# Optimization experiments

Measured on AMD Instinct MI355X. Metric: run time of the kernel, lower is better.

Reference implementation:

```python
import jax, jax.numpy as jnp
import numpy as np
import math

B, S, D = 16, 256, 1024   # batch, seq (= s_model), d_model
HP, HC = 16, 8
DK, SK = D // HP, S // HC
EPS = 1e-6


def setup_inputs() -> dict:
    key = jax.random.key(0)
    ks = jax.random.split(key, 3)
    x = jax.random.normal(ks[0], (B, S, D), dtype=jnp.float32)
    Wp = jax.random.normal(ks[1], (3, D, D), dtype=jnp.float32) * 0.02  # (in,out)
    bp = jnp.zeros((3, D), dtype=jnp.float32)
    Wc = jax.random.normal(ks[2], (4, S, S), dtype=jnp.float32) * 0.02  # (in,out)
    bc = jnp.zeros((4, S), dtype=jnp.float32)
    a_p = jnp.ones((D,), dtype=jnp.float32)
    b_p = jnp.zeros((D,), dtype=jnp.float32)
    a_c = jnp.ones((S,), dtype=jnp.float32)
    b_c = jnp.zeros((S,), dtype=jnp.float32)
    return {"x": x, "Wp": Wp, "bp": bp, "Wc": Wc, "bc": bc,
            "a_p": a_p, "b_p": b_p, "a_c": a_c, "b_c": b_c}


def _std(x, axis):
    # torch .std(): unbiased (ddof=1)
    return jnp.std(x, axis=axis, keepdims=True, ddof=1)


def _attn(q, k, v):
    # q,k,v: [B, H, T, dk]; dropout is identity (eval)
    scores = jnp.einsum('bhtd,bhsd->bhts', q, k) / math.sqrt(q.shape[-1])
    p = jax.nn.softmax(scores, axis=-1)
    return jnp.einsum('bhts,bhsd->bhtd', p, v)


def reference(x, Wp, bp, Wc, bc, a_p, b_p, a_c, b_c):
    nb = x.shape[0]
    # ---- LayerNorm over channels (norm_p) ----
    mean = jnp.mean(x, axis=-1, keepdims=True)
    xp = a_p * (x - mean) / (_std(x, -1) + EPS) + b_p            # [B,S,D]
    # ---- positional attention over sequence ----
    qkv = jnp.einsum('bsd,nde->nbse', xp, Wp) + bp[:, None, None, :]
    q, k, v = [t.reshape(nb, S, HP, DK).transpose(0, 2, 1, 3) for t in qkv]
    xp = _attn(q, k, v).transpose(0, 2, 1, 3).reshape(nb, S, D)  # [B,S,D]
    # ---- LayerNorm_C: stats over sequence dim, affine indexed by seq ----
    mean_c = jnp.mean(xp, axis=-2, keepdims=True)                # [B,1,D]
    xc = a_c[:, None] * (xp - mean_c) / (_std(xp, -2) + EPS) + b_c[:, None]
    # ---- channel attention: channels are tokens, head dim SK ----
    xt = xc.transpose(0, 2, 1)                                    # [B,D,S]
    qkvc = jnp.einsum('bds,nse->nbde', xt, Wc[:3]) + bc[:3, None, None, :]
    qc, kc, vc = [t.reshape(nb, D, HC, SK).transpose(0, 2, 1, 3) for t in qkvc]
    xcatt = _attn(qc, kc, vc).transpose(0, 2, 1, 3).reshape(nb, D, S)  # [B,D,S]
    out = jnp.einsum('bds,se->bde', xcatt, Wc[3]) + bc[3]         # [B,D,S]
    return out.transpose(0, 2, 1)                                  # [B,S,D]
```

## Files before the change

### kernel.cpp

```cpp
#include <hip/hip_runtime.h>
#include <hip/hip_bf16.h>
#include <math.h>

#define B_ 16
#define S_ 256
#define D_ 1024
#define HP_ 16
#define DK_ 64
#define HC_ 8
#define SK_ 32
#define EPS_ 1e-6f

#define ALPHA_P 0.42466089973135876f
#define ALPHA_C 0.50500991942f

typedef __attribute__((ext_vector_type(8))) short short8v;
typedef __attribute__((ext_vector_type(4))) float f32x4;

__device__ __forceinline__ float bf2f(unsigned short h) {
    return __uint_as_float((unsigned)h << 16);
}
__device__ __forceinline__ ushort2 f2bf2(float a, float b) {
    __hip_bfloat162 h = __float22bfloat162_rn(make_float2(a, b));
    union { __hip_bfloat162 h2; ushort2 u2; } cv;
    cv.h2 = h;
    return cv.u2;
}
__device__ __forceinline__ float exp2_fast(float x) {
    float r;
    asm("v_exp_f32 %0, %1\n\ts_nop 0" : "=v"(r) : "v"(x));
    return r;
}
__device__ __forceinline__ void ldlds16(const unsigned short* g, unsigned short* l) {
    const unsigned int* gp = reinterpret_cast<const unsigned int*>(g);
    auto* lp = reinterpret_cast<__attribute__((address_space(3))) unsigned int*>(
        reinterpret_cast<uintptr_t>(l));
    __builtin_amdgcn_global_load_lds(gp, lp, 16, 0, 0);
}

__global__ __launch_bounds__(256) void k1_ln_p(
    const float* __restrict__ x, const float* __restrict__ a_p,
    const float* __restrict__ b_p, unsigned short* __restrict__ xh,
    unsigned short* __restrict__ xl)
{
    const int row = blockIdx.x;
    const float4* xr = (const float4*)(x + (size_t)row * D_);
    const int tid = threadIdx.x;
    float4 v = xr[tid];
    float s  = v.x + v.y + v.z + v.w;
    float sq = v.x*v.x + v.y*v.y + v.z*v.z + v.w*v.w;
    #pragma unroll
    for (int off = 32; off > 0; off >>= 1) {
        s  += __shfl_down(s, off);
        sq += __shfl_down(sq, off);
    }
    __shared__ float red[8];
    const int wid = tid >> 6, lane = tid & 63;
    if (lane == 0) { red[wid] = s; red[4 + wid] = sq; }
    __syncthreads();
    if (tid == 0) {
        float S0 = red[0] + red[1] + red[2] + red[3];
        float Q0 = red[4] + red[5] + red[6] + red[7];
        float mean = S0 / (float)D_;
        float var  = fmaxf((Q0 - (float)D_ * mean * mean) / (float)(D_ - 1), 0.0f);
        red[0] = mean;
        red[1] = 1.0f / (sqrtf(var) + EPS_);
    }
    __syncthreads();
    const float mean = red[0], inv = red[1];
    float4 a = ((const float4*)a_p)[tid];
    float4 b = ((const float4*)b_p)[tid];
    float o0 = a.x * (v.x - mean) * inv + b.x;
    float o1 = a.y * (v.y - mean) * inv + b.y;
    float o2 = a.z * (v.z - mean) * inv + b.z;
    float o3 = a.w * (v.w - mean) * inv + b.w;
    ushort2 h01 = f2bf2(o0, o1), h23 = f2bf2(o2, o3);
    ushort2 l01 = f2bf2(o0 - bf2f(h01.x), o1 - bf2f(h01.y));
    ushort2 l23 = f2bf2(o2 - bf2f(h23.x), o3 - bf2f(h23.y));
    ushort4 hv, lv;
    hv.x = h01.x; hv.y = h01.y; hv.z = h23.x; hv.w = h23.y;
    lv.x = l01.x; lv.y = l01.y; lv.z = l23.x; lv.w = l23.y;
    *(ushort4*)&xh[(size_t)row * D_ + tid*4] = hv;
    *(ushort4*)&xl[(size_t)row * D_ + tid*4] = lv;
}

__global__ __launch_bounds__(256) void tsplit(
    const float* __restrict__ W, unsigned short* __restrict__ Th,
    unsigned short* __restrict__ Tl, int K, int N)
{
    const int z = blockIdx.z;
    W  += (size_t)z * K * N;
    Th += (size_t)z * K * N;
    Tl += (size_t)z * K * N;
    const int k0 = blockIdx.x * 64, n0 = blockIdx.y * 64;
    __shared__ float tile[64][65];
    const int ix = threadIdx.x & 63, iy = threadIdx.x >> 6;
    #pragma unroll
    for (int u = 0; u < 16; u++) {
        const int kk = iy*16 + u;
        tile[kk][ix] = W[(size_t)(k0+kk)*N + n0 + ix];
    }
    __syncthreads();
    #pragma unroll
    for (int u = 0; u < 16; u += 2) {
        const int nn0 = iy*16 + u, nn1 = nn0 + 1;
        const float v0 = tile[ix][nn0], v1 = tile[ix][nn1];
        ushort2 h2 = f2bf2(v0, v1);
        ushort2 l2 = f2bf2(v0 - bf2f(h2.x), v1 - bf2f(h2.y));
        Th[(size_t)(n0+nn0)*K + k0 + ix] = h2.x;
        Th[(size_t)(n0+nn1)*K + k0 + ix] = h2.y;
        Tl[(size_t)(n0+nn0)*K + k0 + ix] = l2.x;
        Tl[(size_t)(n0+nn1)*K + k0 + ix] = l2.y;
    }
}

template<int OUTMODE, int Z>
__global__ __launch_bounds__(256) void mm_mfma(
    const unsigned short* __restrict__ Ah, const unsigned short* __restrict__ Al,
    const unsigned short* __restrict__ Bh, const unsigned short* __restrict__ Bl,
    const float* __restrict__ bias, void* __restrict__ Cout1,
    void* __restrict__ Cout2,
    int M, int N, int K, long sB, long sBias, long sC, long loff, int TB,
    float alpha, int zsplit, int zobase, int lognx)
{
    const int nwg = gridDim.x * gridDim.y;
    const int chunk = nwg >> 3;
    const int flat = blockIdx.x + gridDim.x * blockIdx.y;
    const int logical = (flat & 7) * chunk + (flat >> 3);
    const int bx = logical & ((1 << lognx) - 1);
    const int by = logical >> lognx;
    const int n0 = bx * 128, m0 = by * 128;
    __shared__ __align__(16) unsigned short Ash[2][2][128*32];
    __shared__ __align__(16) unsigned short Bsh[2][Z][2][128*32];
    const int tid = threadIdx.x;
    const int wave = tid >> 6, lane = tid & 63;
    const int wm = wave & 1, wn = wave >> 1;
    const int lrow = lane & 15, quad = lane >> 4;
    size_t gaOff[2], gbOff[2];
    int cb[2];
    #pragma unroll
    for (int j = 0; j < 2; j++) {
        const int p = wave*128 + j*64 + lane;
        const int row = p >> 2;
        const int cc = (p & 3) ^ ((row >> 1) & 3);
        gaOff[j] = (size_t)(m0 + row) * K + cc*8;
        gbOff[j] = (size_t)(n0 + row) * K + cc*8;
        cb[j] = (wave*128 + j*64) * 8;
    }
    int aFr[4], bFr[4];
    #pragma unroll
    for (int i = 0; i < 4; i++) {
        const int ra = wm*64 + i*16 + lrow;
        aFr[i] = ((ra << 2) | (quad ^ ((ra >> 1) & 3))) * 8;
        const int rb = wn*64 + i*16 + lrow;
        bFr[i] = ((rb << 2) | (quad ^ ((rb >> 1) & 3))) * 8;
    }
    f32x4 acc[Z][4][4];
    #pragma unroll
    for (int z = 0; z < Z; z++)
        #pragma unroll
        for (int j = 0; j < 4; j++) {
            const float bv = bias[(size_t)(z + zobase) * sBias + n0 + wn*64 + j*16 + lrow];
            #pragma unroll
            for (int i = 0; i < 4; i++) {
                acc[z][i][j][0] = bv; acc[z][i][j][1] = bv;
                acc[z][i][j][2] = bv; acc[z][i][j][3] = bv;
            }
        }
    #pragma unroll
    for (int j = 0; j < 2; j++) {
        ldlds16(Ah + gaOff[j], &Ash[0][0][cb[j]]);
        ldlds16(Al + gaOff[j], &Ash[0][1][cb[j]]);
        #pragma unroll
        for (int z = 0; z < Z; z++) {
            ldlds16(Bh + (size_t)z * sB + gbOff[j], &Bsh[0][z][0][cb[j]]);
            ldlds16(Bl + (size_t)z * sB + gbOff[j], &Bsh[0][z][1][cb[j]]);
        }
    }
    const int NT = K >> 5;
    for (int kt = 0; kt < NT; kt++) {
        const int cur = kt & 1;
        asm volatile("s_waitcnt vmcnt(0)" ::: "memory");
        asm volatile("s_barrier" ::: "memory");
        if (kt + 1 < NT) {
            const int kk = (kt + 1) * 32;
            #pragma unroll
            for (int j = 0; j < 2; j++) {
                ldlds16(Ah + gaOff[j] + kk, &Ash[cur^1][0][cb[j]]);
                ldlds16(Al + gaOff[j] + kk, &Ash[cur^1][1][cb[j]]);
                #pragma unroll
                for (int z = 0; z < Z; z++) {
                    ldlds16(Bh + (size_t)z * sB + gbOff[j] + kk, &Bsh[cur^1][z][0][cb[j]]);
                    ldlds16(Bl + (size_t)z * sB + gbOff[j] + kk, &Bsh[cur^1][z][1][cb[j]]);
                }
            }
        }
        short8v ahf[4], alf[4];
        #pragma unroll
        for (int i = 0; i < 4; i++) {
            ahf[i] = *(const short8v*)&Ash[cur][0][aFr[i]];
            alf[i] = *(const short8v*)&Ash[cur][1][aFr[i]];
        }
        #pragma unroll
        for (int z = 0; z < Z; z++) {
            short8v bhf[4], blf[4];
            #pragma unroll
            for (int j = 0; j < 4; j++) {
                bhf[j] = *(const short8v*)&Bsh[cur][z][0][bFr[j]];
                blf[j] = *(const short8v*)&Bsh[cur][z][1][bFr[j]];
            }
            #pragma unroll
            for (int i = 0; i < 4; i++) {
                #pragma unroll
                for (int j = 0; j < 4; j++) {
                    acc[z][i][j] = __builtin_amdgcn_mfma_f32_16x16x32_bf16(ahf[i], bhf[j], acc[z][i][j], 0, 0, 0);
                    acc[z][i][j] = __builtin_amdgcn_mfma_f32_16x16x32_bf16(ahf[i], blf[j], acc[z][i][j], 0, 0, 0);
                    acc[z][i][j] = __builtin_amdgcn_mfma_f32_16x16x32_bf16(alf[i], bhf[j], acc[z][i][j], 0, 0, 0);
                }
            }
        }
    }
    #pragma unroll
    for (int z = 0; z < Z; z++) {
        const int zeff = z + zobase;
        #pragma unroll
        for (int i = 0; i < 4; i++) {
            const int mrow = m0 + wm*64 + i*16 + quad*4;
            #pragma unroll
            for (int j = 0; j < 4; j++) {
                const int ncol = n0 + wn*64 + j*16 + lrow;
                if (OUTMODE == 1) {
                    if (zeff < zsplit) {
                        unsigned short* Ch = (unsigned short*)Cout1 + (size_t)zeff * sC;
                        unsigned short* Cl = Ch + loff;
                        #pragma unroll
                        for (int r = 0; r < 4; r += 2) {
                            const float v0 = acc[z][i][j][r] * alpha;
                            const float v1 = acc[z][i][j][r+1] * alpha;
                            ushort2 h2 = f2bf2(v0, v1);
                            ushort2 l2 = f2bf2(v0 - bf2f(h2.x), v1 - bf2f(h2.y));
                            Ch[(size_t)(mrow + r    ) * N + ncol] = h2.x;
                            Ch[(size_t)(mrow + r + 1) * N + ncol] = h2.y;
                            Cl[(size_t)(mrow + r    ) * N + ncol] = l2.x;
                            Cl[(size_t)(mrow + r + 1) * N + ncol] = l2.y;
                        }
                    } else {
                        unsigned short* Ch = (unsigned short*)Cout2;
                        unsigned short* Cl = Ch + loff;
                        const int bidx = mrow / TB, t0 = mrow % TB;
                        const size_t ad = (size_t)bidx * N * TB + (size_t)ncol * TB + t0;
                        const float v0 = acc[z][i][j][0], v1 = acc[z][i][j][1];
                        const float v2 = acc[z][i][j][2], v3 = acc[z][i][j][3];
                        ushort2 h01 = f2bf2(v0, v1), h23 = f2bf2(v2, v3);
                        ushort2 l01 = f2bf2(v0 - bf2f(h01.x), v1 - bf2f(h01.y));
                        ushort2 l23 = f2bf2(v2 - bf2f(h23.x), v3 - bf2f(h23.y));
                        ushort4 hv, lv;
                        hv.x = h01.x; hv.y = h01.y; hv.z = h23.x; hv.w = h23.y;
                        lv.x = l01.x; lv.y = l01.y; lv.z = l23.x; lv.w = l23.y;
                        *(ushort4*)&Ch[ad] = hv;
                        *(ushort4*)&Cl[ad] = lv;
                    }
                } else {
                    float* C = (float*)Cout2;
                    const int bidx = mrow / TB, t0 = mrow % TB;
                    f32x4 a4 = acc[z][i][j];
                    *(float4*)&C[((size_t)bidx * N + ncol) * TB + t0] = *(float4*)&a4;
                }
            }
        }
    }
}

__global__ __launch_bounds__(256) void k3_mfma(
    const unsigned short* __restrict__ qh, const unsigned short* __restrict__ ql,
    const unsigned short* __restrict__ kh, const unsigned short* __restrict__ kl,
    const unsigned short* __restrict__ vth, const unsigned short* __restrict__ vtl,
    float* __restrict__ out)
{
    const int flat = blockIdx.x + (blockIdx.y << 2) + (blockIdx.z << 6);
    const int logical = ((flat & 7) << 7) | (flat >> 3);
    const int m0 = (logical & 3) * 64;
    const int h  = (logical >> 2) & 15;
    const int b  = logical >> 6;
    const int hoff = h * DK_;
    const size_t rowb = (size_t)b * S_;
    __shared__ __align__(16) unsigned short Ksh[2][64*64], Ksl[2][64*64];
    __shared__ __align__(16) unsigned short VTh[2][64*64], VTl[2][64*64];
    __shared__ __align__(16) unsigned short Ps[64][72];
    const int tid = threadIdx.x;
    const int w = tid >> 6, lane = tid & 63;
    const int lrow = lane & 15, quad = lane >> 4;
    short8v bqh[2], bql[2];
    #pragma unroll
    for (int ks = 0; ks < 2; ks++) {
        const size_t qb = (rowb + m0 + w*16 + lrow) * D_ + hoff + ks*32 + quad*8;
        bqh[ks] = *(const short8v*)&qh[qb];
        bql[ks] = *(const short8v*)&ql[qb];
    }
    size_t kOff[2], vOff[2];
    int cb[2];
    #pragma unroll
    for (int j = 0; j < 2; j++) {
        const int p = w*128 + j*64 + lane;
        const int row = p >> 3;
        const int cc = (p & 7) ^ (row & 7);
        kOff[j] = (rowb + row) * D_ + hoff + cc*8;
        vOff[j] = ((size_t)b * D_ + hoff + row) * S_ + cc*8;
        cb[j] = (w*128 + j*64) * 8;
    }
    f32x4 o[4] = {};
    float lacc = 0.f;
    #pragma unroll
    for (int j = 0; j < 2; j++) {
        ldlds16(kh  + kOff[j], &Ksh[0][cb[j]]);
        ldlds16(kl  + kOff[j], &Ksl[0][cb[j]]);
        ldlds16(vth + vOff[j], &VTh[0][cb[j]]);
        ldlds16(vtl + vOff[j], &VTl[0][cb[j]]);
    }
    for (int kt = 0; kt < 4; kt++) {
        const int cur = kt & 1;
        asm volatile("s_waitcnt vmcnt(0)" ::: "memory");
        asm volatile("s_barrier" ::: "memory");
        if (kt < 3) {
            const int n01 = (kt + 1) * 64;
            #pragma unroll
            for (int j = 0; j < 2; j++) {
                ldlds16(kh  + kOff[j] + (size_t)n01 * D_, &Ksh[cur^1][cb[j]]);
                ldlds16(kl  + kOff[j] + (size_t)n01 * D_, &Ksl[cur^1][cb[j]]);
                ldlds16(vth + vOff[j] + n01,              &VTh[cur^1][cb[j]]);
                ldlds16(vtl + vOff[j] + n01,              &VTl[cur^1][cb[j]]);
            }
        }
        f32x4 sa[4] = {};
        #pragma unroll
        for (int ks = 0; ks < 2; ks++) {
            #pragma unroll
            for (int jk = 0; jk < 4; jk++) {
                const int r = jk*16 + lrow, c = ks*4 + quad;
                const int off = ((r << 3) | (c ^ (r & 7))) * 8;
                short8v akh = *(const short8v*)&Ksh[cur][off];
                short8v akl = *(const short8v*)&Ksl[cur][off];
                sa[jk] = __builtin_amdgcn_mfma_f32_16x16x32_bf16(akh, bqh[ks], sa[jk], 0, 0, 0);
                sa[jk] = __builtin_amdgcn_mfma_f32_16x16x32_bf16(akl, bqh[ks], sa[jk], 0, 0, 0);
                sa[jk] = __builtin_amdgcn_mfma_f32_16x16x32_bf16(akh, bql[ks], sa[jk], 0, 0, 0);
            }
        }
        #pragma unroll
        for (int jk = 0; jk < 4; jk++) {
            float p0 = exp2_fast(sa[jk][0]);
            float p1 = exp2_fast(sa[jk][1]);
            float p2 = exp2_fast(sa[jk][2]);
            float p3 = exp2_fast(sa[jk][3]);
            lacc += (p0 + p1) + (p2 + p3);
            ushort2 p01 = f2bf2(p0, p1), p23 = f2bf2(p2, p3);
            ushort4 ph;
            ph.x = p01.x; ph.y = p01.y; ph.z = p23.x; ph.w = p23.y;
            *(ushort4*)&Ps[w*16 + lrow][jk*16 + quad*4] = ph;
        }
        #pragma unroll
        for (int ks = 0; ks < 2; ks++) {
            short8v ap = *(const short8v*)&Ps[w*16 + lrow][ks*32 + quad*8];
            #pragma unroll
            for (int nf = 0; nf < 4; nf++) {
                const int r = nf*16 + lrow, c = ks*4 + quad;
                const int off = ((r << 3) | (c ^ (r & 7))) * 8;
                short8v vH = *(const short8v*)&VTh[cur][off];
                short8v vL = *(const short8v*)&VTl[cur][off];
                o[nf] = __builtin_amdgcn_mfma_f32_16x16x32_bf16(ap, vH, o[nf], 0, 0, 0);
                o[nf] = __builtin_amdgcn_mfma_f32_16x16x32_bf16(ap, vL, o[nf], 0, 0, 0);
            }
        }
    }
    lacc += __shfl_xor(lacc, 16);
    lacc += __shfl_xor(lacc, 32);
    #pragma unroll
    for (int r = 0; r < 4; r++) {
        const float linv = 1.0f / __shfl(lacc, quad*4 + r);
        #pragma unroll
        for (int nf = 0; nf < 4; nf++)
            out[(rowb + m0 + w*16 + quad*4 + r) * D_ + hoff + nf*16 + lrow] =
                o[nf][r] * linv;
    }
}

__global__ __launch_bounds__(256) void k6_mfma(
    const unsigned short* __restrict__ qch, const unsigned short* __restrict__ qcl,
    const unsigned short* __restrict__ kch, const unsigned short* __restrict__ kcl,
    const unsigned short* __restrict__ vth, const unsigned short* __restrict__ vtl,
    unsigned short* __restrict__ oh, unsigned short* __restrict__ ol)
{
    const int flat = blockIdx.x + (blockIdx.y << 3) + (blockIdx.z << 6);
    const int logical = ((flat & 7) << 7) | (flat >> 3);
    const int m0 = (logical & 7) << 7;
    const int h  = (logical >> 3) & 7;
    const int b  = logical >> 6;
    const int hoff = h * SK_;
    const size_t rowb = (size_t)b * D_;
    __shared__ __align__(16) unsigned short Ksh[2][64*32], Ksl[2][64*32];
    __shared__ __align__(16) unsigned short VTh[2][32*64], VTl[2][32*64];
    __shared__ __align__(16) unsigned short Ps[128][72];
    const int tid = threadIdx.x;
    const int w = tid >> 6, lane = tid & 63;
    const int lrow = lane & 15, quad = lane >> 4;
    short8v bqh[2], bql[2];
    #pragma unroll
    for (int i = 0; i < 2; i++) {
        const size_t qb = (rowb + m0 + w*32 + i*16 + lrow) * S_ + hoff + quad*8;
        bqh[i] = *(const short8v*)&qch[qb];
        bql[i] = *(const short8v*)&qcl[qb];
    }
    size_t kOff, vOff;
    {
        const int pK = w*64 + lane;
        const int rowK = pK >> 2;
        const int ccK = (pK & 3) ^ ((rowK >> 1) & 3);
        kOff = (rowb + rowK) * S_ + hoff + ccK*8;
        const int pV = w*64 + lane;
        const int rowV = pV >> 3;
        const int ccV = (pV & 7) ^ (rowV & 7);
        vOff = ((size_t)b * S_ + hoff + rowV) * D_ + ccV*8;
    }
    const int cb = w*64*8;
    f32x4 o[2][2] = {};
    float lacc[2] = {0.f, 0.f};
    ldlds16(kch + kOff, &Ksh[0][cb]);
    ldlds16(kcl + kOff, &Ksl[0][cb]);
    ldlds16(vth + vOff, &VTh[0][cb]);
    ldlds16(vtl + vOff, &VTl[0][cb]);
    for (int kt = 0; kt < 16; kt++) {
        const int cur = kt & 1;
        asm volatile("s_waitcnt vmcnt(0)" ::: "memory");
        asm volatile("s_barrier" ::: "memory");
        if (kt < 15) {
            const int n01 = (kt + 1) * 64;
            ldlds16(kch + kOff + (size_t)n01 * S_, &Ksh[cur^1][cb]);
            ldlds16(kcl + kOff + (size_t)n01 * S_, &Ksl[cur^1][cb]);
            ldlds16(vth + vOff + n01,              &VTh[cur^1][cb]);
            ldlds16(vtl + vOff + n01,              &VTl[cur^1][cb]);
        }
        f32x4 sa[2][4] = {};
        #pragma unroll
        for (int jk = 0; jk < 4; jk++) {
            const int r = jk*16 + lrow;
            const int off = ((r << 2) | (quad ^ ((r >> 1) & 3))) * 8;
            short8v akh = *(const short8v*)&Ksh[cur][off];
            short8v akl = *(const short8v*)&Ksl[cur][off];
            #pragma unroll
            for (int i = 0; i < 2; i++) {
                sa[i][jk] = __builtin_amdgcn_mfma_f32_16x16x32_bf16(akh, bqh[i], sa[i][jk], 0, 0, 0);
                sa[i][jk] = __builtin_amdgcn_mfma_f32_16x16x32_bf16(akl, bqh[i], sa[i][jk], 0, 0, 0);
                sa[i][jk] = __builtin_amdgcn_mfma_f32_16x16x32_bf16(akh, bql[i], sa[i][jk], 0, 0, 0);
            }
        }
        #pragma unroll
        for (int i = 0; i < 2; i++)
            #pragma unroll
            for (int jk = 0; jk < 4; jk++) {
                float p0 = exp2_fast(sa[i][jk][0]);
                float p1 = exp2_fast(sa[i][jk][1]);
                float p2 = exp2_fast(sa[i][jk][2]);
                float p3 = exp2_fast(sa[i][jk][3]);
                lacc[i] += (p0 + p1) + (p2 + p3);
                ushort2 p01 = f2bf2(p0, p1), p23 = f2bf2(p2, p3);
                ushort4 ph;
                ph.x = p01.x; ph.y = p01.y; ph.z = p23.x; ph.w = p23.y;
                *(ushort4*)&Ps[w*32 + i*16 + lrow][jk*16 + quad*4] = ph;
            }
        #pragma unroll
        for (int ks = 0; ks < 2; ks++) {
            short8v ap[2];
            #pragma unroll
            for (int i = 0; i < 2; i++)
                ap[i] = *(const short8v*)&Ps[w*32 + i*16 + lrow][ks*32 + quad*8];
            #pragma unroll
            for (int nf = 0; nf < 2; nf++) {
                const int r = nf*16 + lrow, c = ks*4 + quad;
                const int off = ((r << 3) | (c ^ (r & 7))) * 8;
                short8v vHf = *(const short8v*)&VTh[cur][off];
                short8v vLf = *(const short8v*)&VTl[cur][off];
                #pragma unroll
                for (int i = 0; i < 2; i++) {
                    o[i][nf] = __builtin_amdgcn_mfma_f32_16x16x32_bf16(ap[i], vHf, o[i][nf], 0, 0, 0);
                    o[i][nf] = __builtin_amdgcn_mfma_f32_16x16x32_bf16(ap[i], vLf, o[i][nf], 0, 0, 0);
                }
            }
        }
    }
    #pragma unroll
    for (int i = 0; i < 2; i++) {
        lacc[i] += __shfl_xor(lacc[i], 16);
        lacc[i] += __shfl_xor(lacc[i], 32);
    }
    #pragma unroll
    for (int i = 0; i < 2; i++)
        #pragma unroll
        for (int r = 0; r < 4; r++) {
            const float linv = 1.0f / __shfl(lacc[i], quad*4 + r);
            const float v0 = o[i][0][r] * linv;
            const float v1 = o[i][1][r] * linv;
            ushort2 h2 = f2bf2(v0, v1);
            ushort2 l2 = f2bf2(v0 - bf2f(h2.x), v1 - bf2f(h2.y));
            const size_t idx =
                (rowb + m0 + w*32 + i*16 + quad*4 + r) * S_ + hoff + lrow;
            oh[idx]      = h2.x;
            oh[idx + 16] = h2.y;
            ol[idx]      = l2.x;
            ol[idx + 16] = l2.y;
        }
}

__global__ __launch_bounds__(256) void k4_fused(
    const float* __restrict__ x, const float* __restrict__ a_c,
    const float* __restrict__ b_c, unsigned short* __restrict__ xth,
    unsigned short* __restrict__ xtl)
{
    const int d0 = blockIdx.x * 64, b = blockIdx.y;
    __shared__ float tile[256][65];
    __shared__ float part[8][64];
    __shared__ float stats[2][64];
    __shared__ float acs[256], bcs[256];
    const int tid = threadIdx.x;
    acs[tid] = a_c[tid];
    bcs[tid] = b_c[tid];
    const int dl = tid & 63, sq = tid >> 6;
    float s1 = 0.f, s2 = 0.f;
    #pragma unroll 8
    for (int u = 0; u < 64; u++) {
        const int srow = sq*64 + u;
        const float v = x[((size_t)(b*S_ + srow))*D_ + d0 + dl];
        tile[srow][dl] = v;
        s1 += v; s2 += v*v;
    }
    part[sq][dl] = s1; part[4+sq][dl] = s2;
    __syncthreads();
    if (tid < 64) {
        const float S = part[0][tid]+part[1][tid]+part[2][tid]+part[3][tid];
        const float Q = part[4][tid]+part[5][tid]+part[6][tid]+part[7][tid];
        const float mean = S / (float)S_;
        const float var  = fmaxf((Q - (float)S_*mean*mean)/(float)(S_-1), 0.f);
        stats[0][tid] = mean;
        stats[1][tid] = 1.f/(sqrtf(var)+EPS_);
    }
    __syncthreads();
    const int dd = tid >> 2, s00 = (tid & 3) * 64;
    const float mean = stats[0][dd], inv = stats[1][dd];
    const size_t obase = ((size_t)(b*D_ + d0 + dd))*S_ + s00;
    #pragma unroll
    for (int c = 0; c < 8; c++) {
        union { ushort u[8]; uint4 v4; } hb, lb;
        #pragma unroll
        for (int t = 0; t < 8; t += 2) {
            const int s = s00 + c*8 + t;
            const float v0 = acs[s]  *(tile[s][dd]  -mean)*inv + bcs[s];
            const float v1 = acs[s+1]*(tile[s+1][dd]-mean)*inv + bcs[s+1];
            ushort2 h2 = f2bf2(v0, v1);
            ushort2 l2 = f2bf2(v0 - bf2f(h2.x), v1 - bf2f(h2.y));
            hb.u[t] = h2.x; hb.u[t+1] = h2.y;
            lb.u[t] = l2.x; lb.u[t+1] = l2.y;
        }
        *(uint4*)&xth[obase + c*8] = hb.v4;
        *(uint4*)&xtl[obase + c*8] = lb.v4;
    }
}

extern "C" void kernel_launch(void* const* d_in, const int* in_sizes, int n_in,
                              void* d_out, int out_size, void* d_ws, size_t ws_size,
                              hipStream_t stream)
{
    const float* x   = (const float*)d_in[0];
    const float* Wp  = (const float*)d_in[1];
    const float* bp  = (const float*)d_in[2];
    const float* Wc  = (const float*)d_in[3];
    const float* bc  = (const float*)d_in[4];
    const float* a_p = (const float*)d_in[5];
    const float* b_p = (const float*)d_in[6];
    const float* a_c = (const float*)d_in[7];
    const float* b_c = (const float*)d_in[8];
    float* out = (float*)d_out;
    float* ws  = (float*)d_ws;
    const size_t NE = (size_t)B_ * S_ * D_;

    float* S0 = ws;
    float* S1 = ws + NE;
    float* S2 = ws + 2*NE;
    float* S3 = ws + 3*NE;
    unsigned short* SW = (unsigned short*)(ws + 4*NE);

    const size_t baseBytes = 4*NE*sizeof(float);
    const bool big = ws_size >= baseBytes + (size_t)2 * 3 * D_ * D_ * sizeof(unsigned short) * 2;

    unsigned short* xh = (unsigned short*)S0;
    unsigned short* xl = xh + NE;
    unsigned short* q_h  = (unsigned short*)S1;
    unsigned short* k_h  = (unsigned short*)S2;
    unsigned short* vt_h = (unsigned short*)S3;

    k1_ln_p<<<dim3(B_*S_), 256, 0, stream>>>(x, a_p, b_p, xh, xl);

    if (big) {
        unsigned short* WTh = SW;
        unsigned short* WTl = WTh + (size_t)3 * D_ * D_;
        tsplit<<<dim3(D_/64, D_/64, 3), 256, 0, stream>>>(Wp, WTh, WTl, D_, D_);
        mm_mfma<1,3><<<dim3(D_/128, (B_*S_)/128), 256, 0, stream>>>(
            xh, xl, WTh, WTl, bp, (void*)q_h, (void*)vt_h,
            B_*S_, D_, D_, (long)D_*D_, (long)D_, (long)(2*NE), (long)NE, S_,
            ALPHA_P, 2, 0, 3);
    } else {
        unsigned short* WTh = SW;
        unsigned short* WTl = WTh + (size_t)D_ * D_;
        for (int z = 0; z < 3; z++) {
            tsplit<<<dim3(D_/64, D_/64, 1), 256, 0, stream>>>(
                Wp + (size_t)z*D_*D_, WTh, WTl, D_, D_);
            mm_mfma<1,1><<<dim3(D_/128, (B_*S_)/128), 256, 0, stream>>>(
                xh, xl, WTh, WTl, bp, (void*)q_h, (void*)vt_h,
                B_*S_, D_, D_, 0, (long)D_, (long)(2*NE), (long)NE, S_,
                ALPHA_P, 2, z, 3);
        }
    }

    k3_mfma<<<dim3(S_/64, HP_, B_), 256, 0, stream>>>(
        q_h, q_h + NE, k_h, k_h + NE, vt_h, vt_h + NE, S0);

    unsigned short* xth = (unsigned short*)S1;
    k4_fused<<<dim3(D_/64, B_), 256, 0, stream>>>(S0, a_c, b_c, xth, xth + NE);

    unsigned short* WcTh = SW;
    unsigned short* WcTl = WcTh + (size_t)4 * S_ * S_;
    tsplit<<<dim3(S_/64, S_/64, 4), 256, 0, stream>>>(Wc, WcTh, WcTl, S_, S_);
    unsigned short* qc_h  = (unsigned short*)S2;
    unsigned short* vct_h = (unsigned short*)S0;
    mm_mfma<1,3><<<dim3(S_/128, (B_*D_)/128), 256, 0, stream>>>(
        xth, xth + NE, WcTh, WcTl, bc, (void*)qc_h, (void*)vct_h,
        B_*D_, S_, S_, (long)S_*S_, (long)S_, (long)(2*NE), (long)NE, D_,
        ALPHA_C, 2, 0, 1);

    unsigned short* kc_h = (unsigned short*)S3;
    unsigned short* xch  = (unsigned short*)S1;
    k6_mfma<<<dim3(D_/128, HC_, B_), 256, 0, stream>>>(
        qc_h, qc_h + NE, kc_h, kc_h + NE, vct_h, vct_h + NE, xch, xch + NE);

    mm_mfma<3,1><<<dim3(S_/128, (B_*D_)/128), 256, 0, stream>>>(
        xch, xch + NE, WcTh + (size_t)3*S_*S_, WcTl + (size_t)3*S_*S_, bc + 3*S_,
        nullptr, (void*)out, B_*D_, S_, S_, 0, 0, 0, 0, D_, 1.0f, 0, 0, 1);
}
```

Before: 307.0 us.

## Shrink GEMM N-tile to 64 with 1D grid and two-block occupancy

Changes the split-bf16 MFMA GEMM tile from 128x128 to 128x64 and launches it on a flat 1D grid of 512 workgroups with XCD-aware remapping. It adds a launch bound that asks for two blocks per CU, shrinks the B shared-memory buffer, and reorders the inner loop so B fragments for all Z outputs are loaded first and A fragments are streamed per row block. The aim is to double the workgroup count for better CU fill on the small GEMMs and to raise occupancy. In exchange there is less reuse of A per tile and more A traffic from global memory.

```diff
diff --git a/kernel.cpp b/kernel.cpp
--- a/kernel.cpp
+++ b/kernel.cpp
@@ -115,7 +115,7 @@
 }
 
 template<int OUTMODE, int Z>
-__global__ __launch_bounds__(256) void mm_mfma(
+__global__ __launch_bounds__(256, 2) void mm_z(
     const unsigned short* __restrict__ Ah, const unsigned short* __restrict__ Al,
     const unsigned short* __restrict__ Bh, const unsigned short* __restrict__ Bl,
     const float* __restrict__ bias, void* __restrict__ Cout1,
@@ -123,103 +123,106 @@
     int M, int N, int K, long sB, long sBias, long sC, long loff, int TB,
     float alpha, int zsplit, int zobase, int lognx)
 {
-    const int nwg = gridDim.x * gridDim.y;
+    const int nwg = gridDim.x;
     const int chunk = nwg >> 3;
-    const int flat = blockIdx.x + gridDim.x * blockIdx.y;
+    const int flat = blockIdx.x;
     const int logical = (flat & 7) * chunk + (flat >> 3);
     const int bx = logical & ((1 << lognx) - 1);
     const int by = logical >> lognx;
-    const int n0 = bx * 128, m0 = by * 128;
+    const int n0 = bx * 64, m0 = by * 128;
     __shared__ __align__(16) unsigned short Ash[2][2][128*32];
-    __shared__ __align__(16) unsigned short Bsh[2][Z][2][128*32];
+    __shared__ __align__(16) unsigned short Bsh[2][Z][2][64*32];
     const int tid = threadIdx.x;
     const int wave = tid >> 6, lane = tid & 63;
     const int wm = wave & 1, wn = wave >> 1;
     const int lrow = lane & 15, quad = lane >> 4;
-    size_t gaOff[2], gbOff[2];
-    int cb[2];
+    size_t gaOff[2];
+    int cbA[2];
     #pragma unroll
     for (int j = 0; j < 2; j++) {
-        const int p = wave*128 + j*64 + lane;
+        const int p = j*256 + tid;
         const int row = p >> 2;
         const int cc = (p & 3) ^ ((row >> 1) & 3);
         gaOff[j] = (size_t)(m0 + row) * K + cc*8;
-        gbOff[j] = (size_t)(n0 + row) * K + cc*8;
-        cb[j] = (wave*128 + j*64) * 8;
-    }
-    int aFr[4], bFr[4];
+        cbA[j] = (j*256 + wave*64) * 8;
+    }
+    size_t gbOff;
+    int cbB;
+    {
+        const int row = tid >> 2;
+        const int cc = (tid & 3) ^ ((row >> 1) & 3);
+        gbOff = (size_t)(n0 + row) * K + cc*8;
+        cbB = (wave*64) * 8;
+    }
+    int aFr[4], bFr[2];
     #pragma unroll
     for (int i = 0; i < 4; i++) {
         const int ra = wm*64 + i*16 + lrow;
         aFr[i] = ((ra << 2) | (quad ^ ((ra >> 1) & 3))) * 8;
-        const int rb = wn*64 + i*16 + lrow;
-        bFr[i] = ((rb << 2) | (quad ^ ((rb >> 1) & 3))) * 8;
-    }
-    f32x4 acc[Z][4][4];
+    }
+    #pragma unroll
+    for (int j = 0; j < 2; j++) {
+        const int rb = wn*32 + j*16 + lrow;
+        bFr[j] = ((rb << 2) | (quad ^ ((rb >> 1) & 3))) * 8;
+    }
+    f32x4 acc[Z][4][2];
     #pragma unroll
     for (int z = 0; z < Z; z++)
         #pragma unroll
-        for (int j = 0; j < 4; j++) {
-            const float bv = bias[(size_t)(z + zobase) * sBias + n0 + wn*64 + j*16 + lrow];
+        for (int j = 0; j < 2; j++) {
+            const float bv = bias[(size_t)(z + zobase) * sBias + n0 + wn*32 + j*16 + lrow];
             #pragma unroll
             for (int i = 0; i < 4; i++) {
                 acc[z][i][j][0] = bv; acc[z][i][j][1] = bv;
                 acc[z][i][j][2] = bv; acc[z][i][j][3] = bv;
             }
         }
-    #pragma unroll
-    for (int j = 0; j < 2; j++) {
-        ldlds16(Ah + gaOff[j], &Ash[0][0][cb[j]]);
-        ldlds16(Al + gaOff[j], &Ash[0][1][cb[j]]);
-        #pragma unroll
-        for (int z = 0; z < Z; z++) {
-            ldlds16(Bh + (size_t)z * sB + gbOff[j], &Bsh[0][z][0][cb[j]]);
-            ldlds16(Bl + (size_t)z * sB + gbOff[j], &Bsh[0][z][1][cb[j]]);
-        }
-    }
+    #define STAGEZ(t, buf)                                                     \
+        {                                                                      \
+            const int kk_ = (t) * 32;                                          \
+            _Pragma("unroll")                                                  \
+            for (int j = 0; j < 2; j++) {                                      \
+                ldlds16(Ah + gaOff[j] + kk_, &Ash[buf][0][cbA[j]]);            \
+                ldlds16(Al + gaOff[j] + kk_, &Ash[buf][1][cbA[j]]);            \
+            }                                                                  \
+            _Pragma("unroll")                                                  \
+            for (int z = 0; z < Z; z++) {                                      \
+                ldlds16(Bh + (size_t)z * sB + gbOff + kk_, &Bsh[buf][z][0][cbB]); \
+                ldlds16(Bl + (size_t)z * sB + gbOff + kk_, &Bsh[buf][z][1][cbB]); \
+            }                                                                  \
+        }
     const int NT = K >> 5;
+    STAGEZ(0, 0)
     for (int kt = 0; kt < NT; kt++) {
         const int cur = kt & 1;
         asm volatile("s_waitcnt vmcnt(0)" ::: "memory");
         asm volatile("s_barrier" ::: "memory");
-        if (kt + 1 < NT) {
-            const int kk = (kt + 1) * 32;
+        if (kt + 1 < NT)
+            STAGEZ(kt + 1, cur ^ 1)
+        short8v bhf[Z][2], blf[Z][2];
+        #pragma unroll
+        for (int z = 0; z < Z; z++)
             #pragma unroll
             for (int j = 0; j < 2; j++) {
-                ldlds16(Ah + gaOff[j] + kk, &Ash[cur^1][0][cb[j]]);
-                ldlds16(Al + gaOff[j] + kk, &Ash[cur^1][1][cb[j]]);
+                bhf[z][j] = *(const short8v*)&Bsh[cur][z][0][bFr[j]];
+                blf[z][j] = *(const short8v*)&Bsh[cur][z][1][bFr[j]];
+            }
+        #pragma unroll
+        for (int i = 0; i < 4; i++) {
+            short8v ahf = *(const short8v*)&Ash[cur][0][aFr[i]];
+            short8v alf = *(const short8v*)&Ash[cur][1][aFr[i]];
+            #pragma unroll
+            for (int z = 0; z < Z; z++) {
                 #pragma unroll
-                for (int z = 0; z < Z; z++) {
-                    ldlds16(Bh + (size_t)z * sB + gbOff[j] + kk, &Bsh[cur^1][z][0][cb[j]]);
-                    ldlds16(Bl + (size_t)z * sB + gbOff[j] + kk, &Bsh[cur^1][z][1][cb[j]]);
+                for (int j = 0; j < 2; j++) {
+                    acc[z][i][j] = __builtin_amdgcn_mfma_f32_16x16x32_bf16(ahf, bhf[z][j], acc[z][i][j], 0, 0, 0);
+                    acc[z][i][j] = __builtin_amdgcn_mfma_f32_16x16x32_bf16(ahf, blf[z][j], acc[z][i][j], 0, 0, 0);
+                    acc[z][i][j] = __builtin_amdgcn_mfma_f32_16x16x32_bf16(alf, bhf[z][j], acc[z][i][j], 0, 0, 0);
                 }
             }
         }
-        short8v ahf[4], alf[4];
-        #pragma unroll
-        for (int i = 0; i < 4; i++) {
-            ahf[i] = *(const short8v*)&Ash[cur][0][aFr[i]];
-            alf[i] = *(const short8v*)&Ash[cur][1][aFr[i]];
-        }
-        #pragma unroll
-        for (int z = 0; z < Z; z++) {
-            short8v bhf[4], blf[4];
-            #pragma unroll
-            for (int j = 0; j < 4; j++) {
-                bhf[j] = *(const short8v*)&Bsh[cur][z][0][bFr[j]];
-                blf[j] = *(const short8v*)&Bsh[cur][z][1][bFr[j]];
-            }
-            #pragma unroll
-            for (int i = 0; i < 4; i++) {
-                #pragma unroll
-                for (int j = 0; j < 4; j++) {
-                    acc[z][i][j] = __builtin_amdgcn_mfma_f32_16x16x32_bf16(ahf[i], bhf[j], acc[z][i][j], 0, 0, 0);
-                    acc[z][i][j] = __builtin_amdgcn_mfma_f32_16x16x32_bf16(ahf[i], blf[j], acc[z][i][j], 0, 0, 0);
-                    acc[z][i][j] = __builtin_amdgcn_mfma_f32_16x16x32_bf16(alf[i], bhf[j], acc[z][i][j], 0, 0, 0);
-                }
-            }
-        }
-    }
+    }
+    #undef STAGEZ
     #pragma unroll
     for (int z = 0; z < Z; z++) {
         const int zeff = z + zobase;
@@ -227,8 +230,8 @@
         for (int i = 0; i < 4; i++) {
             const int mrow = m0 + wm*64 + i*16 + quad*4;
             #pragma unroll
-            for (int j = 0; j < 4; j++) {
-                const int ncol = n0 + wn*64 + j*16 + lrow;
+            for (int j = 0; j < 2; j++) {
+                const int ncol = n0 + wn*32 + j*16 + lrow;
                 if (OUTMODE == 1) {
                     if (zeff < zsplit) {
                         unsigned short* Ch = (unsigned short*)Cout1 + (size_t)zeff * sC;
@@ -601,20 +604,20 @@
         unsigned short* WTh = SW;
         unsigned short* WTl = WTh + (size_t)3 * D_ * D_;
         tsplit<<<dim3(D_/64, D_/64, 3), 256, 0, stream>>>(Wp, WTh, WTl, D_, D_);
-        mm_mfma<1,3><<<dim3(D_/128, (B_*S_)/128), 256, 0, stream>>>(
+        mm_z<1,3><<<dim3(512), 256, 0, stream>>>(
             xh, xl, WTh, WTl, bp, (void*)q_h, (void*)vt_h,
             B_*S_, D_, D_, (long)D_*D_, (long)D_, (long)(2*NE), (long)NE, S_,
-            ALPHA_P, 2, 0, 3);
+            ALPHA_P, 2, 0, 4);
     } else {
         unsigned short* WTh = SW;
         unsigned short* WTl = WTh + (size_t)D_ * D_;
         for (int z = 0; z < 3; z++) {
             tsplit<<<dim3(D_/64, D_/64, 1), 256, 0, stream>>>(
                 Wp + (size_t)z*D_*D_, WTh, WTl, D_, D_);
-            mm_mfma<1,1><<<dim3(D_/128, (B_*S_)/128), 256, 0, stream>>>(
+            mm_z<1,1><<<dim3(512), 256, 0, stream>>>(
                 xh, xl, WTh, WTl, bp, (void*)q_h, (void*)vt_h,
                 B_*S_, D_, D_, 0, (long)D_, (long)(2*NE), (long)NE, S_,
-                ALPHA_P, 2, z, 3);
+                ALPHA_P, 2, z, 4);
         }
     }
 
@@ -629,17 +632,17 @@
     tsplit<<<dim3(S_/64, S_/64, 4), 256, 0, stream>>>(Wc, WcTh, WcTl, S_, S_);
     unsigned short* qc_h  = (unsigned short*)S2;
     unsigned short* vct_h = (unsigned short*)S0;
-    mm_mfma<1,3><<<dim3(S_/128, (B_*D_)/128), 256, 0, stream>>>(
+    mm_z<1,3><<<dim3(512), 256, 0, stream>>>(
         xth, xth + NE, WcTh, WcTl, bc, (void*)qc_h, (void*)vct_h,
         B_*D_, S_, S_, (long)S_*S_, (long)S_, (long)(2*NE), (long)NE, D_,
-        ALPHA_C, 2, 0, 1);
+        ALPHA_C, 2, 0, 2);
 
     unsigned short* kc_h = (unsigned short*)S3;
     unsigned short* xch  = (unsigned short*)S1;
     k6_mfma<<<dim3(D_/128, HC_, B_), 256, 0, stream>>>(
         qc_h, qc_h + NE, kc_h, kc_h + NE, vct_h, vct_h + NE, xch, xch + NE);
 
-    mm_mfma<3,1><<<dim3(S_/128, (B_*D_)/128), 256, 0, stream>>>(
+    mm_z<3,1><<<dim3(512), 256, 0, stream>>>(
         xch, xch + NE, WcTh + (size_t)3*S_*S_, WcTl + (size_t)3*S_*S_, bc + 3*S_,
-        nullptr, (void*)out, B_*D_, S_, S_, 0, 0, 0, 0, D_, 1.0f, 0, 0, 1);
-}
+        nullptr, (void*)out, B_*D_, S_, S_, 0, 0, 0, 0, D_, 1.0f, 0, 0, 2);
+}
```

Result: faster. 285.8 us (median of 3 runs) (-6.9%).
